# Optimization experiments

Hardware: AMD Instinct MI355X
Metric: run time of the kernel (lower is better)

## Reference

```python
import jax, jax.numpy as jnp
import numpy as np
import math

B, S, DIM = 2, 2048, 2048
H = 16
NOPE, ROPE = 96, 32
HD = 128          # head_dim = NOPE + ROPE
KVR, QR = 512, 1536


def _rope_tables():
    inv_freq = 1.0 / (10000.0 ** (np.arange(0, ROPE, 2, dtype=np.float32) / ROPE))  # [ROPE/2]
    t = np.arange(S, dtype=np.float32)
    freqs = np.outer(t, inv_freq)  # [S, ROPE/2]
    return jnp.asarray(np.cos(freqs)), jnp.asarray(np.sin(freqs))


def setup_inputs() -> dict:
    key = jax.random.key(0)
    ks = jax.random.split(key, 8)
    w = 0.02
    cos, sin = _rope_tables()
    return {
        "x": jax.random.normal(ks[0], (B, S, DIM), jnp.float32),
        "freqs_cos": cos,
        "freqs_sin": sin,
        "wq_down": jax.random.normal(ks[1], (DIM, QR), jnp.float32) * w,
        "wq_up": jax.random.normal(ks[2], (QR, H * HD), jnp.float32) * w,
        "wkv_down": jax.random.normal(ks[3], (DIM, KVR), jnp.float32) * w,
        "w_up_nope": jax.random.normal(ks[4], (KVR, H * NOPE), jnp.float32) * w,
        "w_up_rope": jax.random.normal(ks[5], (KVR, H * ROPE), jnp.float32) * w,
        "w_up_val": jax.random.normal(ks[6], (KVR, H * HD), jnp.float32) * w,
        "wo": jax.random.normal(ks[7], (H * HD, DIM), jnp.float32) * w,
    }


def _apply_rope(x, cos, sin):
    # x: [B, S, H, D_r]; cos/sin: [S, D_r/2]
    xr = x[..., 0::2]
    xi = x[..., 1::2]
    c = cos[None, :, None, :]
    s = sin[None, :, None, :]
    out_r = xr * c - xi * s
    out_i = xr * s + xi * c
    return jnp.stack([out_r, out_i], axis=-1).reshape(x.shape)


def reference(x, freqs_cos, freqs_sin, wq_down, wq_up, wkv_down,
              w_up_nope, w_up_rope, w_up_val, wo):
    b, s, _ = x.shape
    # Q path: low-rank down then up
    q = (x @ wq_down) @ wq_up                 # [B,S,H*HD]
    q = q.reshape(b, s, H, HD)
    q_nope, q_rope = q[..., :NOPE], q[..., NOPE:]
    q_rope = _apply_rope(q_rope, freqs_cos, freqs_sin)

    # KV path: shared latent
    kv_latent = x @ wkv_down                  # [B,S,KVR]
    k_nope = (kv_latent @ w_up_nope).reshape(b, s, H, NOPE)
    k_rope = _apply_rope((kv_latent @ w_up_rope).reshape(b, s, H, ROPE),
                         freqs_cos, freqs_sin)
    v = (kv_latent @ w_up_val).reshape(b, s, H, HD)

    q_final = jnp.concatenate([q_nope, q_rope], axis=-1)   # [B,S,H,HD]
    k_final = jnp.concatenate([k_nope, k_rope], axis=-1)

    scores = jnp.einsum("bqhd,bkhd->bhqk", q_final, k_final) / math.sqrt(HD)
    causal = jnp.tril(jnp.ones((s, s), dtype=bool))        # [S,S]
    scores = jnp.where(causal[None, None], scores, -jnp.inf)
    attn = jax.nn.softmax(scores, axis=-1)
    out = jnp.einsum("bhqk,bkhd->bqhd", attn, v).reshape(b, s, H * HD)
    return out @ wo
```

## Files before the change

### kernel.cpp

```cpp
#include <hip/hip_runtime.h>
#include <hip/hip_bf16.h>
#include <stdint.h>

#define B_    2
#define S_    2048
#define DIM_  2048
#define H_    16
#define NOPE_ 96
#define ROPE_ 32
#define HD_   128
#define KVR_  512
#define QR_   1536
#define BS_   (B_*S_)
#define NQT_  (S_/128)

typedef __bf16 bf16_t;
typedef bf16_t bf16x8 __attribute__((ext_vector_type(8)));
typedef float  f32x4  __attribute__((ext_vector_type(4)));

__device__ __forceinline__ uint16_t f2bf(float f) {
  union { float f; uint32_t u; } v; v.f = f;
  uint32_t r = (v.u + 0x7fffu + ((v.u >> 16) & 1u)) >> 16;
  return (uint16_t)r;
}
__device__ __forceinline__ uint32_t pk_bf16(float a, float b) {
  union { float f; uint32_t u; } x, y; x.f = a; y.f = b;
  uint32_t lo = (x.u + 0x7fffu + ((x.u >> 16) & 1u)) >> 16;
  uint32_t hi = (y.u + 0x7fffu + ((y.u >> 16) & 1u)) & 0xffff0000u;
  return hi | lo;
}

__device__ __forceinline__ void gl_lds16(const void* g, void* l) {
  __builtin_amdgcn_global_load_lds(
      (const __attribute__((address_space(1))) uint32_t*)g,
      (__attribute__((address_space(3))) uint32_t*)l, 16, 0, 0);
}

__device__ __forceinline__ void transpose_tile(const float* __restrict__ W,
                                               uint16_t* __restrict__ Wt,
                                               int K, int N, float scale, int lbid,
                                               float (*tile)[65]) {
  const int nb = N / 64;
  const int n0 = (lbid % nb) * 64, k0 = (lbid / nb) * 64;
  const int tid = threadIdx.x;
  #pragma unroll
  for (int i = 0; i < 4; i++) {
    int p = i * 256 + tid;
    int r = p >> 4, c4 = (p & 15) * 4;
    float4 v = *(const float4*)&W[(size_t)(k0 + r) * N + n0 + c4];
    tile[r][c4 + 0] = v.x; tile[r][c4 + 1] = v.y; tile[r][c4 + 2] = v.z; tile[r][c4 + 3] = v.w;
  }
  __syncthreads();
  #pragma unroll
  for (int i = 0; i < 4; i++) {
    int p = i * 256 + tid;
    int rn = p >> 4, c4 = (p & 15) * 4;
    ushort4 o;
    o.x = f2bf(tile[c4 + 0][rn] * scale); o.y = f2bf(tile[c4 + 1][rn] * scale);
    o.z = f2bf(tile[c4 + 2][rn] * scale); o.w = f2bf(tile[c4 + 3][rn] * scale);
    *(ushort4*)&Wt[(size_t)(n0 + rn) * K + k0 + c4] = o;
  }
}

#define CAST_BLKS 2048
__global__ __launch_bounds__(256) void prep_k(
    const float* __restrict__ x,
    const float* __restrict__ wqd, const float* __restrict__ wqu,
    const float* __restrict__ wkvd, const float* __restrict__ wn,
    const float* __restrict__ wr, const float* __restrict__ wv,
    const float* __restrict__ wo,
    uint16_t* __restrict__ xb, uint16_t* __restrict__ wdT,
    uint16_t* __restrict__ wquT, uint16_t* __restrict__ wkrT,
    uint16_t* __restrict__ wvT, uint16_t* __restrict__ woT, float qscale) {
  __shared__ __align__(16) float tile[64][65];
  int bid = blockIdx.x;
  const int tid = threadIdx.x;
  if (bid < CAST_BLKS) {
    #pragma unroll
    for (int p = 0; p < 4; p++) {
      int i = bid * 4096 + p * 1024 + tid * 4;
      float4 v = *(const float4*)&x[i];
      ushort4 o; o.x = f2bf(v.x); o.y = f2bf(v.y); o.z = f2bf(v.z); o.w = f2bf(v.w);
      *(ushort4*)&xb[i] = o;
    }
    return;
  }
  bid -= CAST_BLKS;
  if (bid < 768)               transpose_tile(wqd,  wdT,                        2048, 1536, 1.f,    bid, tile);
  else if ((bid -= 768) < 256) transpose_tile(wkvd, wdT + (size_t)QR_ * DIM_,   2048,  512, 1.f,    bid, tile);
  else if ((bid -= 256) < 768) transpose_tile(wqu,  wquT,                       1536, 2048, qscale, bid, tile);
  else if ((bid -= 768) < 192) transpose_tile(wn,   wkrT,                        512, 1536, 1.f,    bid, tile);
  else if ((bid -= 192) < 64)  transpose_tile(wr,   wkrT + (size_t)1536 * 512,   512,  512, 1.f,    bid, tile);
  else if ((bid -= 64) < 256)  transpose_tile(wv,   wvT,                         512, 2048, 1.f,    bid, tile);
  else                         transpose_tile(wo,   woT, 2048, 2048, 1.f, bid - 256, tile);
}
#define PREP_BLKS (CAST_BLKS + 768 + 256 + 768 + 192 + 64 + 256 + 1024)

template<int MODE>
__global__ __launch_bounds__(256) void gemm_bt(const uint16_t* __restrict__ A,
                                               const uint16_t* __restrict__ Bt,
                                               void* __restrict__ C,
                                               int M, int N, int K,
                                               int lda, int ldb, int ldc,
                                               const float* __restrict__ cos_t,
                                               const float* __restrict__ sin_t) {
  __shared__ __align__(16) uint16_t As[128][64];
  __shared__ __align__(16) uint16_t Bs[128][64];
  const int tid = threadIdx.x;
  const int wave = tid >> 6, lane = tid & 63;
  const int wm = wave & 1, wn = wave >> 1;
  const int m0 = blockIdx.y * 128, n0 = blockIdx.x * 128;
  const int fr = lane & 15, fq = lane >> 4;

  f32x4 acc[4][4] = {};

  const int srow = wave * 32 + (lane >> 3);
  const int sg   = ((lane & 7) ^ ((lane >> 3) & 7));
  const int scol = sg * 8;

  for (int k0 = 0; k0 < K; k0 += 64) {
    #pragma unroll
    for (int i = 0; i < 4; i++) {
      gl_lds16(A  + (size_t)(m0 + srow + i * 8) * lda + k0 + scol, &As[wave * 32 + i * 8][0]);
      gl_lds16(Bt + (size_t)(n0 + srow + i * 8) * ldb + k0 + scol, &Bs[wave * 32 + i * 8][0]);
    }
    __syncthreads();
    #pragma unroll
    for (int ks = 0; ks < 2; ks++) {
      bf16x8 af[4], bf[4];
      #pragma unroll
      for (int mt = 0; mt < 4; mt++) {
        int pc = (ks * 4 + fq) ^ (fr & 7);
        af[mt] = *(const bf16x8*)&As[wm * 64 + mt * 16 + fr][pc * 8];
      }
      #pragma unroll
      for (int nt = 0; nt < 4; nt++) {
        int pc = (ks * 4 + fq) ^ (fr & 7);
        bf[nt] = *(const bf16x8*)&Bs[wn * 64 + nt * 16 + fr][pc * 8];
      }
      #pragma unroll
      for (int mt = 0; mt < 4; mt++)
        #pragma unroll
        for (int nt = 0; nt < 4; nt++)
          acc[mt][nt] = __builtin_amdgcn_mfma_f32_16x16x32_bf16(bf[nt], af[mt], acc[mt][nt], 0, 0, 0);
    }
    __syncthreads();
  }
  #pragma unroll
  for (int mt = 0; mt < 4; mt++) {
    const int gm = m0 + wm * 64 + mt * 16 + fr;
    #pragma unroll
    for (int nt = 0; nt < 4; nt++) {
      const int gn = n0 + wn * 64 + nt * 16 + fq * 4;
      f32x4 a = acc[mt][nt];
      if (MODE == 0) {
        ushort4 o; o.x = f2bf(a[0]); o.y = f2bf(a[1]); o.z = f2bf(a[2]); o.w = f2bf(a[3]);
        *(ushort4*)&((uint16_t*)C)[(size_t)gm * ldc + gn] = o;
      } else if (MODE == 1) {
        float4 o; o.x = a[0]; o.y = a[1]; o.z = a[2]; o.w = a[3];
        *(float4*)&((float*)C)[(size_t)gm * ldc + gn] = o;
      } else if (MODE == 2) {
        int d = gn & 127;
        if (d >= 96) {
          int s = gm & (S_ - 1);
          int i0 = (d - 96) >> 1;
          float c0 = cos_t[s * 16 + i0],     s0 = sin_t[s * 16 + i0];
          float c1 = cos_t[s * 16 + i0 + 1], s1 = sin_t[s * 16 + i0 + 1];
          float r0 = a[0] * c0 - a[1] * s0, r1 = a[0] * s0 + a[1] * c0;
          float r2 = a[2] * c1 - a[3] * s1, r3 = a[2] * s1 + a[3] * c1;
          a[0] = r0; a[1] = r1; a[2] = r2; a[3] = r3;
        }
        ushort4 o; o.x = f2bf(a[0]); o.y = f2bf(a[1]); o.z = f2bf(a[2]); o.w = f2bf(a[3]);
        *(ushort4*)&((uint16_t*)C)[(size_t)gm * ldc + gn] = o;
      } else {
        int dstcol;
        if (gn < 1536) {
          int h = gn / 96;
          dstcol = h * 128 + (gn - h * 96);
        } else {
          int ln = gn - 1536;
          int h = ln >> 5, dd = ln & 31;
          int s = gm & (S_ - 1);
          int i0 = dd >> 1;
          float c0 = cos_t[s * 16 + i0],     s0 = sin_t[s * 16 + i0];
          float c1 = cos_t[s * 16 + i0 + 1], s1 = sin_t[s * 16 + i0 + 1];
          float r0 = a[0] * c0 - a[1] * s0, r1 = a[0] * s0 + a[1] * c0;
          float r2 = a[2] * c1 - a[3] * s1, r3 = a[2] * s1 + a[3] * c1;
          a[0] = r0; a[1] = r1; a[2] = r2; a[3] = r3;
          dstcol = h * 128 + 96 + dd;
        }
        ushort4 o; o.x = f2bf(a[0]); o.y = f2bf(a[1]); o.z = f2bf(a[2]); o.w = f2bf(a[3]);
        *(ushort4*)&((uint16_t*)C)[(size_t)gm * 2048 + dstcol] = o;
      }
    }
  }
}

__global__ __launch_bounds__(512) void attn_kernel(const uint16_t* __restrict__ Q,
                                                   const uint16_t* __restrict__ Kf,
                                                   const uint16_t* __restrict__ Vt,
                                                   uint16_t* __restrict__ O) {
  __shared__ __align__(16) uint16_t Ks[64][128];
  __shared__ __align__(16) uint16_t Vs[128][64];
  __shared__ __align__(16) uint16_t Ps[8][16][72];
  const int bid = blockIdx.x;
  const int idx = bid & 255;
  const int qt = (bid >> 8) ? (idx >> 5) : (NQT_ - 1 - (idx >> 5));
  const int hb = idx & 31;
  const int h = hb >> 1, b = hb & 1;
  const int tid = threadIdx.x, wave = tid >> 6, lane = tid & 63;
  const int fr = lane & 15, fq = lane >> 4;
  const int q0 = qt * 128;
  const int qrow = q0 + wave * 16;

  bf16x8 qf[4];
  const uint16_t* qbase = Q + (size_t)(b * S_ + qrow + fr) * (H_ * HD_) + h * HD_ + fq * 8;
  #pragma unroll
  for (int s4 = 0; s4 < 4; s4++) qf[s4] = *(const bf16x8*)(qbase + s4 * 32);

  float l_s = 0.f;
  f32x4 oacc[8] = {};

  const int ksrow_lo = wave * 4 + (lane >> 4);
  const int kg_chunk0 = (lane & 15);
  const int vsrow_lo = wave * 8 + (lane >> 3);
  const int vg_chunk = (lane & 7) ^ ((lane >> 3) & 7);

  const int nkt = 2 * qt + 2;
  for (int kt = 0; kt < nkt; kt++) {
    #pragma unroll
    for (int i = 0; i < 2; i++) {
      int row = i * 32 + ksrow_lo;
      int g = kg_chunk0 ^ (row & 15);
      gl_lds16(Kf + (size_t)(b * S_ + kt * 64 + row) * (H_ * HD_) + h * HD_ + g * 8,
               &Ks[i * 32 + wave * 4][0]);
    }
    #pragma unroll
    for (int i = 0; i < 2; i++) {
      int row = i * 64 + vsrow_lo;
      gl_lds16(Vt + (size_t)(h * HD_ + row) * BS_ + b * S_ + kt * 64 + vg_chunk * 8,
               &Vs[i * 64 + wave * 8][0]);
    }
    __syncthreads();

    if (kt * 64 <= qrow + 15) {
      f32x4 sacc[4] = {};
      #pragma unroll
      for (int ks = 0; ks < 4; ks++) {
        int pc = (ks * 4 + fq) ^ fr;
        #pragma unroll
        for (int nt = 0; nt < 4; nt++) {
          bf16x8 kfr = *(const bf16x8*)&Ks[nt * 16 + fr][pc * 8];
          sacc[nt] = __builtin_amdgcn_mfma_f32_16x16x32_bf16(kfr, qf[ks], sacc[nt], 0, 0, 0);
        }
      }
      const bool need_mask = (kt * 64 + 63 > qrow);
      const int qg = qrow + fr;
      #pragma unroll
      for (int nt = 0; nt < 4; nt++) {
        float p[4];
        #pragma unroll
        for (int r = 0; r < 4; r++) {
          float pp = __builtin_amdgcn_exp2f(sacc[nt][r]);
          if (need_mask) {
            int kg = kt * 64 + nt * 16 + fq * 4 + r;
            if (kg > qg) pp = 0.f;
          }
          l_s += pp;
          p[r] = pp;
        }
        uint2 w; w.x = pk_bf16(p[0], p[1]); w.y = pk_bf16(p[2], p[3]);
        *(uint2*)&Ps[wave][fr][nt * 16 + fq * 4] = w;
      }
      #pragma unroll
      for (int ks = 0; ks < 2; ks++) {
        bf16x8 pf = *(const bf16x8*)&Ps[wave][fr][ks * 32 + fq * 8];
        int pc = (ks * 4 + fq) ^ (fr & 7);
        #pragma unroll
        for (int d = 0; d < 8; d++) {
          bf16x8 vf = *(const bf16x8*)&Vs[d * 16 + fr][pc * 8];
          oacc[d] = __builtin_amdgcn_mfma_f32_16x16x32_bf16(vf, pf, oacc[d], 0, 0, 0);
        }
      }
    }
    __syncthreads();
  }
  l_s += __shfl_xor(l_s, 16);
  l_s += __shfl_xor(l_s, 32);
  const float inv_l = 1.0f / l_s;
  const int gm = b * S_ + qrow + fr;
  #pragma unroll
  for (int dt = 0; dt < 8; dt++) {
    ushort4 o;
    o.x = f2bf(oacc[dt][0] * inv_l); o.y = f2bf(oacc[dt][1] * inv_l);
    o.z = f2bf(oacc[dt][2] * inv_l); o.w = f2bf(oacc[dt][3] * inv_l);
    *(ushort4*)&O[(size_t)gm * (H_ * HD_) + h * HD_ + dt * 16 + fq * 4] = o;
  }
}

extern "C" void kernel_launch(void* const* d_in, const int* in_sizes, int n_in,
                              void* d_out, int out_size, void* d_ws, size_t ws_size,
                              hipStream_t stream) {
  const float* x        = (const float*)d_in[0];
  const float* fcos     = (const float*)d_in[1];
  const float* fsin     = (const float*)d_in[2];
  const float* wq_down  = (const float*)d_in[3];
  const float* wq_up    = (const float*)d_in[4];
  const float* wkv_down = (const float*)d_in[5];
  const float* w_nope   = (const float*)d_in[6];
  const float* w_rope   = (const float*)d_in[7];
  const float* w_val    = (const float*)d_in[8];
  const float* wo       = (const float*)d_in[9];
  float* out = (float*)d_out;

  char* ws = (char*)d_ws;
  size_t off = 0;
  auto alloc = [&](size_t elems) {
    uint16_t* p = (uint16_t*)(ws + off);
    off += elems * 2; off = (off + 255) & ~(size_t)255;
    return p;
  };
  uint16_t* xb     = alloc((size_t)BS_ * DIM_);
  uint16_t* wdT    = alloc((size_t)(QR_ + KVR_) * DIM_);
  uint16_t* wquT   = alloc((size_t)(H_ * HD_) * QR_);
  uint16_t* wkrT   = alloc((size_t)(H_ * NOPE_ + H_ * ROPE_) * KVR_);
  uint16_t* wvT    = alloc((size_t)(H_ * HD_) * KVR_);
  uint16_t* woT    = alloc((size_t)DIM_ * (H_ * HD_));
  uint16_t* latcat = alloc((size_t)BS_ * (QR_ + KVR_));
  uint16_t* qbuf   = alloc((size_t)BS_ * (H_ * HD_));
  uint16_t* kfin   = alloc((size_t)BS_ * (H_ * HD_));
  uint16_t* vTb    = alloc((size_t)(H_ * HD_) * BS_);
  uint16_t* aout   = alloc((size_t)BS_ * (H_ * HD_));

  const float qscale = 0.12751743f;

  prep_k<<<dim3(PREP_BLKS), 256, 0, stream>>>(x, wq_down, wq_up, wkv_down, w_nope,
      w_rope, w_val, wo, xb, wdT, wquT, wkrT, wvT, woT, qscale);

  gemm_bt<0><<<dim3(2048 / 128, BS_ / 128), 256, 0, stream>>>(xb, wdT, latcat,
      BS_, 2048, DIM_, DIM_, DIM_, 2048, nullptr, nullptr);
  gemm_bt<2><<<dim3((H_ * HD_) / 128, BS_ / 128), 256, 0, stream>>>(latcat, wquT, qbuf,
      BS_, H_ * HD_, QR_, 2048, QR_, H_ * HD_, fcos, fsin);
  gemm_bt<3><<<dim3(2048 / 128, BS_ / 128), 256, 0, stream>>>(latcat + QR_, wkrT, kfin,
      BS_, 2048, KVR_, 2048, KVR_, 2048, fcos, fsin);
  gemm_bt<0><<<dim3(BS_ / 128, (H_ * HD_) / 128), 256, 0, stream>>>(wvT, latcat + QR_, vTb,
      H_ * HD_, BS_, KVR_, KVR_, 2048, BS_, nullptr, nullptr);

  attn_kernel<<<dim3(NQT_ * H_ * B_), 512, 0, stream>>>(qbuf, kfin, vTb, aout);
  gemm_bt<1><<<dim3(DIM_ / 128, BS_ / 128), 256, 0, stream>>>(aout, woT, out,
      BS_, DIM_, DIM_, DIM_, DIM_, DIM_, nullptr, nullptr);
}
```

Measured before the change: 374.6 us.

## Merge Q, K, and V up-projection GEMMs into one launch; reorder attention tiles

Factors the GEMM body into a device function and adds one kernel that dispatches 1536 blocks across the Q-up (with rope), K-up (with rope), and V-transposed GEMMs. This replaces three launches, removing launch gaps and the tail idle time between kernels. The attention block order also changes to a single heaviest-first causal ordering instead of the two-half interleave. The new order may change load balance across CUs, and the merged kernel's register use is set by the largest branch.

```diff
diff --git a/kernel.cpp b/kernel.cpp
--- a/kernel.cpp
+++ b/kernel.cpp
@@ -97,19 +97,18 @@
 #define PREP_BLKS (CAST_BLKS + 768 + 256 + 768 + 192 + 64 + 256 + 1024)
 
 template<int MODE>
-__global__ __launch_bounds__(256) void gemm_bt(const uint16_t* __restrict__ A,
-                                               const uint16_t* __restrict__ Bt,
-                                               void* __restrict__ C,
-                                               int M, int N, int K,
-                                               int lda, int ldb, int ldc,
-                                               const float* __restrict__ cos_t,
-                                               const float* __restrict__ sin_t) {
-  __shared__ __align__(16) uint16_t As[128][64];
-  __shared__ __align__(16) uint16_t Bs[128][64];
+__device__ __forceinline__ void gemm_body(const uint16_t* __restrict__ A,
+                                          const uint16_t* __restrict__ Bt,
+                                          void* __restrict__ C,
+                                          int bx, int by, int K,
+                                          int lda, int ldb, int ldc,
+                                          const float* __restrict__ cos_t,
+                                          const float* __restrict__ sin_t,
+                                          uint16_t (*As)[64], uint16_t (*Bs)[64]) {
   const int tid = threadIdx.x;
   const int wave = tid >> 6, lane = tid & 63;
   const int wm = wave & 1, wn = wave >> 1;
-  const int m0 = blockIdx.y * 128, n0 = blockIdx.x * 128;
+  const int m0 = by * 128, n0 = bx * 128;
   const int fr = lane & 15, fq = lane >> 4;
 
   f32x4 acc[4][4] = {};
@@ -196,6 +195,43 @@
   }
 }
 
+template<int MODE>
+__global__ __launch_bounds__(256) void gemm_bt(const uint16_t* __restrict__ A,
+                                               const uint16_t* __restrict__ Bt,
+                                               void* __restrict__ C,
+                                               int K, int lda, int ldb, int ldc) {
+  __shared__ __align__(16) uint16_t As[128][64];
+  __shared__ __align__(16) uint16_t Bs[128][64];
+  gemm_body<MODE>(A, Bt, C, blockIdx.x, blockIdx.y, K, lda, ldb, ldc,
+                  nullptr, nullptr, As, Bs);
+}
+
+__global__ __launch_bounds__(256) void up3_k(const uint16_t* __restrict__ latcat,
+                                             const uint16_t* __restrict__ wquT,
+                                             const uint16_t* __restrict__ wkrT,
+                                             const uint16_t* __restrict__ wvT,
+                                             uint16_t* __restrict__ qbuf,
+                                             uint16_t* __restrict__ kfin,
+                                             uint16_t* __restrict__ vTb,
+                                             const float* __restrict__ cos_t,
+                                             const float* __restrict__ sin_t) {
+  __shared__ __align__(16) uint16_t As[128][64];
+  __shared__ __align__(16) uint16_t Bs[128][64];
+  int bid = blockIdx.x;
+  if (bid < 512) {
+    gemm_body<2>(latcat, wquT, qbuf, bid & 15, bid >> 4, QR_, 2048, QR_, 2048,
+                 cos_t, sin_t, As, Bs);
+  } else if (bid < 1024) {
+    bid -= 512;
+    gemm_body<3>(latcat + QR_, wkrT, kfin, bid & 15, bid >> 4, KVR_, 2048, KVR_, 2048,
+                 cos_t, sin_t, As, Bs);
+  } else {
+    bid -= 1024;
+    gemm_body<0>(wvT, latcat + QR_, vTb, bid & 31, bid >> 5, KVR_, KVR_, 2048, BS_,
+                 nullptr, nullptr, As, Bs);
+  }
+}
+
 __global__ __launch_bounds__(512) void attn_kernel(const uint16_t* __restrict__ Q,
                                                    const uint16_t* __restrict__ Kf,
                                                    const uint16_t* __restrict__ Vt,
@@ -204,9 +240,8 @@
   __shared__ __align__(16) uint16_t Vs[128][64];
   __shared__ __align__(16) uint16_t Ps[8][16][72];
   const int bid = blockIdx.x;
-  const int idx = bid & 255;
-  const int qt = (bid >> 8) ? (idx >> 5) : (NQT_ - 1 - (idx >> 5));
-  const int hb = idx & 31;
+  const int qt = (NQT_ - 1) - (bid / (H_ * B_));
+  const int hb = bid % (H_ * B_);
   const int h = hb >> 1, b = hb & 1;
   const int tid = threadIdx.x, wave = tid >> 6, lane = tid & 63;
   const int fr = lane & 15, fq = lane >> 4;
@@ -338,15 +373,11 @@
       w_rope, w_val, wo, xb, wdT, wquT, wkrT, wvT, woT, qscale);
 
   gemm_bt<0><<<dim3(2048 / 128, BS_ / 128), 256, 0, stream>>>(xb, wdT, latcat,
-      BS_, 2048, DIM_, DIM_, DIM_, 2048, nullptr, nullptr);
-  gemm_bt<2><<<dim3((H_ * HD_) / 128, BS_ / 128), 256, 0, stream>>>(latcat, wquT, qbuf,
-      BS_, H_ * HD_, QR_, 2048, QR_, H_ * HD_, fcos, fsin);
-  gemm_bt<3><<<dim3(2048 / 128, BS_ / 128), 256, 0, stream>>>(latcat + QR_, wkrT, kfin,
-      BS_, 2048, KVR_, 2048, KVR_, 2048, fcos, fsin);
-  gemm_bt<0><<<dim3(BS_ / 128, (H_ * HD_) / 128), 256, 0, stream>>>(wvT, latcat + QR_, vTb,
-      H_ * HD_, BS_, KVR_, KVR_, 2048, BS_, nullptr, nullptr);
+      DIM_, DIM_, DIM_, 2048);
+  up3_k<<<dim3(1536), 256, 0, stream>>>(latcat, wquT, wkrT, wvT, qbuf, kfin, vTb,
+      fcos, fsin);
 
   attn_kernel<<<dim3(NQT_ * H_ * B_), 512, 0, stream>>>(qbuf, kfin, vTb, aout);
   gemm_bt<1><<<dim3(DIM_ / 128, BS_ / 128), 256, 0, stream>>>(aout, woT, out,
-      BS_, DIM_, DIM_, DIM_, DIM_, DIM_, nullptr, nullptr);
-}
+      DIM_, DIM_, DIM_, DIM_);
+}
```

New measurement: 357.4 us. -4.6%, faster.
